# Performance work log

Measured on AMD Instinct MI355X. Metric: run time of the kernel, lower is better.

Reference implementation:

```python
import jax, jax.numpy as jnp
import numpy as np

OUT = 400          # resize target (tf.image.resize(img, [400, 400]))
THRESH = 0.7       # default threshold_value
B, H, W, C = 32, 512, 512, 3


def setup_inputs() -> dict:
    key = jax.random.key(0)
    k1, k2 = jax.random.split(key)
    image = jax.random.normal(k1, (B, H, W, C), dtype=jnp.float32)
    tensor = jax.random.uniform(k2, (B, H, W, 1), dtype=jnp.float32)
    return {"image": image, "tensor": tensor}


def _bounds(nz):
    # nz: bool [N]; first/last True index (tf.where(...)[0][0], [-1][0])
    n = nz.shape[0]
    first = jnp.argmax(nz).astype(jnp.int32)
    last = (n - 1 - jnp.argmax(nz[::-1])).astype(jnp.int32)
    return first, last


def _axis_coords(lo, hi, out):
    # TF2 bilinear resize: half-pixel centers, clamp into [0, size-1].
    # Crop is img[lo:hi] (exclusive hi, matching the TF slice semantics).
    size = (hi - lo).astype(jnp.float32)
    src = (jnp.arange(out, dtype=jnp.float32) + 0.5) * size / out - 0.5
    src = jnp.clip(src, 0.0, jnp.maximum(size - 1.0, 0.0))
    i0 = jnp.floor(src).astype(jnp.int32)
    i1 = jnp.minimum(i0 + 1, jnp.maximum(hi - lo - 1, 0))
    w = src - i0.astype(jnp.float32)
    return lo + i0, lo + i1, w  # absolute indices into the full image


def _crop_resize(img, msk):
    # img: [H, W, C]; msk: bool [H, W] == (tensor[..., 0] > THRESH)
    # rows: sum over axis=1 (tf sum_of_col), cols: sum over axis=0 (tf sum_of_row)
    left, right = _bounds(jnp.any(msk, axis=1))
    top, bot = _bounds(jnp.any(msk, axis=0))
    r0, r1, wr = _axis_coords(left, right, OUT)
    c0, c1, wc = _axis_coords(top, bot, OUT)
    a00 = img[r0[:, None], c0[None, :], :]
    a01 = img[r0[:, None], c1[None, :], :]
    a10 = img[r1[:, None], c0[None, :], :]
    a11 = img[r1[:, None], c1[None, :], :]
    wr_ = wr[:, None, None]
    wc_ = wc[None, :, None]
    top_i = a00 * (1.0 - wc_) + a01 * wc_
    bot_i = a10 * (1.0 - wc_) + a11 * wc_
    return top_i * (1.0 - wr_) + bot_i * wr_  # [OUT, OUT, C]


def reference(image, tensor):
    mask = tensor[..., 0] > THRESH
    return jax.vmap(_crop_resize)(image, mask)  # [B, 400, 400, C]
```

## Files before the change

kernel.cpp:

```cpp
#include <hip/hip_runtime.h>

#define OUTN 400
#define THRESH 0.7f
#define BB 32
#define HH 512
#define WW 512
#define CC 3
#define BIGI 0x7FFFFFFF

#define CHUNKS_PB 32
#define ROWS_PC   (HH / CHUNKS_PB)
#define PXPB      (OUTN * OUTN)
#define TPB       320
#define PXB       (TPB * 2)
#define BLKS_PB   (PXPB / PXB)
#define NXCD      8
#define RGRID     (BB * BLKS_PB)

typedef float vfloat4 __attribute__((ext_vector_type(4)));

__global__ void __launch_bounds__(256) bounds_part_kernel(
        const float* __restrict__ tensor,
        int4* __restrict__ part) {
    const int task  = blockIdx.x;
    const int b     = task >> 5;
    const int chunk = task & 31;

    const vfloat4* base = (const vfloat4*)(tensor + (size_t)b * HH * WW
                                                  + (size_t)chunk * ROWS_PC * WW);

    int minR = BIGI, maxR = -1, minC = BIGI, maxC = -1;

    #pragma unroll
    for (int it = 0; it < 8; ++it) {
        int p = threadIdx.x + it * 256;
        vfloat4 v = __builtin_nontemporal_load(base + p);
        int row  = p >> 7;
        int col0 = (p & 127) * 4;
        int mask = (v.x > THRESH ? 1 : 0) | (v.y > THRESH ? 2 : 0)
                 | (v.z > THRESH ? 4 : 0) | (v.w > THRESH ? 8 : 0);
        if (mask) {
            minR = min(minR, row);
            maxR = max(maxR, row);
            minC = min(minC, col0 + __builtin_ctz(mask));
            maxC = max(maxC, col0 + (31 - __builtin_clz(mask)));
        }
    }

    #pragma unroll
    for (int off = 32; off > 0; off >>= 1) {
        minR = min(minR, __shfl_down(minR, off));
        maxR = max(maxR, __shfl_down(maxR, off));
        minC = min(minC, __shfl_down(minC, off));
        maxC = max(maxC, __shfl_down(maxC, off));
    }

    __shared__ int s[4];
    if (threadIdx.x == 0) { s[0] = BIGI; s[1] = -1; s[2] = BIGI; s[3] = -1; }
    __syncthreads();
    if ((threadIdx.x & 63) == 0) {
        atomicMin(&s[0], minR); atomicMax(&s[1], maxR);
        atomicMin(&s[2], minC); atomicMax(&s[3], maxC);
    }
    __syncthreads();
    if (threadIdx.x == 0) {
        int4 r;
        if (s[1] >= 0) {
            r.x = s[0] + chunk * ROWS_PC;
            r.y = s[1] + chunk * ROWS_PC;
            r.z = s[2];
            r.w = s[3];
        } else {
            r.x = BIGI; r.y = -1; r.z = BIGI; r.w = -1;
        }
        part[task] = r;
    }
}

__device__ inline int4 fold_bounds(const int4* __restrict__ part, int b, int lane) {
    int4 p = part[b * CHUNKS_PB + (lane & 31)];
    #pragma unroll
    for (int off = 1; off < 32; off <<= 1) {
        p.x = min(p.x, __shfl_xor(p.x, off));
        p.y = max(p.y, __shfl_xor(p.y, off));
        p.z = min(p.z, __shfl_xor(p.z, off));
        p.w = max(p.w, __shfl_xor(p.w, off));
    }
    if (p.y < 0) { p.x = 0; p.y = HH - 1; }
    if (p.w < 0) { p.z = 0; p.w = WW - 1; }
    return p;
}

__device__ inline void ld3(const float* __restrict__ p, float* d) {
    d[0] = p[0]; d[1] = p[1]; d[2] = p[2];
}

__global__ void __launch_bounds__(TPB) resize_kernel(
        const float* __restrict__ img,
        const int4* __restrict__ part,
        float* __restrict__ out) {
    const int logical = (blockIdx.x % NXCD) * (RGRID / NXCD) + blockIdx.x / NXCD;

    const int t    = threadIdx.x;
    const int b    = logical / BLKS_PB;
    const int rem  = (logical % BLKS_PB) * PXB + t * 2;
    const int lane = t & 63;

    int4 f = fold_bounds(part, b, lane);
    const int minR = f.x, maxR = f.y, minC = f.z, maxC = f.w;

    const int ocol = rem % OUTN;
    const int orow = rem / OUTN;

    float sizeR = (float)(maxR - minR);
    float srcR  = ((float)orow + 0.5f) * sizeR * (1.0f / OUTN) - 0.5f;
    srcR = fminf(fmaxf(srcR, 0.0f), fmaxf(sizeR - 1.0f, 0.0f));
    int   i0 = (int)floorf(srcR);
    int   i1 = min(i0 + 1, max(maxR - minR - 1, 0));
    float wr = srcR - (float)i0;
    const int ro0 = (minR + i0) * (WW * CC);
    const int ro1 = (minR + i1) * (WW * CC);

    const float sizeC  = (float)(maxC - minC);
    const float hiClip = fmaxf(sizeC - 1.0f, 0.0f);
    const int   jmax   = max(maxC - minC - 1, 0);

    float srcC0 = ((float)ocol + 0.5f) * sizeC * (1.0f / OUTN) - 0.5f;
    srcC0 = fminf(fmaxf(srcC0, 0.0f), hiClip);
    int   j00 = (int)floorf(srcC0);
    int   j01 = min(j00 + 1, jmax);
    float wc0 = srcC0 - (float)j00;
    const int c00 = (minC + j00) * CC, c01 = (minC + j01) * CC;

    float srcC1 = ((float)ocol + 1.5f) * sizeC * (1.0f / OUTN) - 0.5f;
    srcC1 = fminf(fmaxf(srcC1, 0.0f), hiClip);
    int   j10 = (int)floorf(srcC1);
    int   j11 = min(j10 + 1, jmax);
    float wc1 = srcC1 - (float)j10;
    const int c10 = (minC + j10) * CC, c11 = (minC + j11) * CC;

    const float* __restrict__ ib = img + (size_t)b * (HH * WW * CC);

    float a00[3], a01[3], a10[3], a11[3];
    float d00[3], d01[3], d10[3], d11[3];
    ld3(ib + ro0 + c00, a00);
    ld3(ib + ro0 + c01, a01);
    ld3(ib + ro1 + c00, a10);
    ld3(ib + ro1 + c01, a11);
    ld3(ib + ro0 + c10, d00);
    ld3(ib + ro0 + c11, d01);
    ld3(ib + ro1 + c10, d10);
    ld3(ib + ro1 + c11, d11);

    float res[6];
    {
        float omc = 1.0f - wc0, omr = 1.0f - wr;
        #pragma unroll
        for (int ch = 0; ch < CC; ++ch) {
            float top = a00[ch] * omc + a01[ch] * wc0;
            float bot = a10[ch] * omc + a11[ch] * wc0;
            res[ch] = top * omr + bot * wr;
        }
        omc = 1.0f - wc1;
        #pragma unroll
        for (int ch = 0; ch < CC; ++ch) {
            float top = d00[ch] * omc + d01[ch] * wc1;
            float bot = d10[ch] * omc + d11[ch] * wc1;
            res[3 + ch] = top * omr + bot * wr;
        }
    }

    float* o = out + ((size_t)b * PXPB + (size_t)rem) * CC;
    #pragma unroll
    for (int i = 0; i < 6; ++i)
        __builtin_nontemporal_store(res[i], o + i);
}

extern "C" void kernel_launch(void* const* d_in, const int* in_sizes, int n_in,
                              void* d_out, int out_size, void* d_ws, size_t ws_size,
                              hipStream_t stream) {
    const float* image  = (const float*)d_in[0];
    const float* tensor = (const float*)d_in[1];
    float* out  = (float*)d_out;
    int4*  part = (int4*)d_ws;

    hipLaunchKernelGGL(bounds_part_kernel, dim3(BB * CHUNKS_PB), dim3(256), 0, stream,
                       tensor, part);

    hipLaunchKernelGGL(resize_kernel, dim3(RGRID), dim3(TPB), 0, stream,
                       image, part, out);
}
```

Baseline: 39.73 us.

## Stage source rows in LDS and compute row bands per block

The resize kernel now gives each block a band of 4 output rows. The block first cooperatively copies the 6 source image rows that band needs into shared memory with vector loads, and each thread then produces 5 consecutive output pixels from LDS. This replaces scattered per-pixel global gathers with coalesced row loads plus LDS reads, aiming to cut redundant global and L2 traffic. In exchange it adds a block-wide barrier, uses about 36 KB of LDS per block, which limits occupancy, and always loads full-width rows even when the crop is narrow.

```diff
diff --git a/kernel.cpp b/kernel.cpp
--- a/kernel.cpp
+++ b/kernel.cpp
@@ -12,10 +12,12 @@
 #define ROWS_PC   (HH / CHUNKS_PB)
 #define PXPB      (OUTN * OUTN)
 #define TPB       320
-#define PXB       (TPB * 2)
-#define BLKS_PB   (PXPB / PXB)
+#define ROWS_PBLK 4
+#define BANDS_PB  (OUTN / ROWS_PBLK)
+#define RGRID     (BB * BANDS_PB)
 #define NXCD      8
-#define RGRID     (BB * BLKS_PB)
+#define SROWS     6
+#define ROWF      (WW * CC)
 
 typedef float vfloat4 __attribute__((ext_vector_type(4)));
 
@@ -91,88 +93,75 @@
     return p;
 }
 
-__device__ inline void ld3(const float* __restrict__ p, float* d) {
-    d[0] = p[0]; d[1] = p[1]; d[2] = p[2];
-}
-
 __global__ void __launch_bounds__(TPB) resize_kernel(
         const float* __restrict__ img,
         const int4* __restrict__ part,
         float* __restrict__ out) {
     const int logical = (blockIdx.x % NXCD) * (RGRID / NXCD) + blockIdx.x / NXCD;
+    const int t     = threadIdx.x;
+    const int b     = logical / BANDS_PB;
+    const int orow0 = (logical % BANDS_PB) * ROWS_PBLK;
 
-    const int t    = threadIdx.x;
-    const int b    = logical / BLKS_PB;
-    const int rem  = (logical % BLKS_PB) * PXB + t * 2;
-    const int lane = t & 63;
-
-    int4 f = fold_bounds(part, b, lane);
+    int4 f = fold_bounds(part, b, t & 63);
     const int minR = f.x, maxR = f.y, minC = f.z, maxC = f.w;
 
-    const int ocol = rem % OUTN;
-    const int orow = rem / OUTN;
+    const float sizeR  = (float)(maxR - minR);
+    const float hiClpR = fmaxf(sizeR - 1.0f, 0.0f);
+    const int   imaxR  = max(maxR - minR - 1, 0);
 
-    float sizeR = (float)(maxR - minR);
-    float srcR  = ((float)orow + 0.5f) * sizeR * (1.0f / OUTN) - 0.5f;
-    srcR = fminf(fmaxf(srcR, 0.0f), fmaxf(sizeR - 1.0f, 0.0f));
+    float s0 = ((float)orow0 + 0.5f) * sizeR / (float)OUTN - 0.5f;
+    s0 = fminf(fmaxf(s0, 0.0f), hiClpR);
+    int rstart = minR + (int)floorf(s0);
+    rstart = min(rstart, HH - SROWS);
+
+    __shared__ float lds[SROWS * ROWF];
+
+    {
+        const vfloat4* src = (const vfloat4*)(img + (size_t)b * (HH * ROWF)
+                                                  + (size_t)rstart * ROWF);
+        vfloat4* dst = (vfloat4*)lds;
+        for (int p = t; p < SROWS * (ROWF / 4); p += TPB)
+            dst[p] = src[p];
+    }
+    __syncthreads();
+
+    const int row   = orow0 + t / 80;
+    const int ocol0 = (t % 80) * 5;
+
+    float srcR = ((float)row + 0.5f) * sizeR / (float)OUTN - 0.5f;
+    srcR = fminf(fmaxf(srcR, 0.0f), hiClpR);
     int   i0 = (int)floorf(srcR);
-    int   i1 = min(i0 + 1, max(maxR - minR - 1, 0));
+    int   i1 = min(i0 + 1, imaxR);
     float wr = srcR - (float)i0;
-    const int ro0 = (minR + i0) * (WW * CC);
-    const int ro1 = (minR + i1) * (WW * CC);
+    const float* __restrict__ row0 = lds + (size_t)(minR + i0 - rstart) * ROWF;
+    const float* __restrict__ row1 = lds + (size_t)(minR + i1 - rstart) * ROWF;
+    const float omr = 1.0f - wr;
 
     const float sizeC  = (float)(maxC - minC);
-    const float hiClip = fmaxf(sizeC - 1.0f, 0.0f);
-    const int   jmax   = max(maxC - minC - 1, 0);
+    const float hiClpC = fmaxf(sizeC - 1.0f, 0.0f);
+    const int   jmaxC  = max(maxC - minC - 1, 0);
 
-    float srcC0 = ((float)ocol + 0.5f) * sizeC * (1.0f / OUTN) - 0.5f;
-    srcC0 = fminf(fmaxf(srcC0, 0.0f), hiClip);
-    int   j00 = (int)floorf(srcC0);
-    int   j01 = min(j00 + 1, jmax);
-    float wc0 = srcC0 - (float)j00;
-    const int c00 = (minC + j00) * CC, c01 = (minC + j01) * CC;
-
-    float srcC1 = ((float)ocol + 1.5f) * sizeC * (1.0f / OUTN) - 0.5f;
-    srcC1 = fminf(fmaxf(srcC1, 0.0f), hiClip);
-    int   j10 = (int)floorf(srcC1);
-    int   j11 = min(j10 + 1, jmax);
-    float wc1 = srcC1 - (float)j10;
-    const int c10 = (minC + j10) * CC, c11 = (minC + j11) * CC;
-
-    const float* __restrict__ ib = img + (size_t)b * (HH * WW * CC);
-
-    float a00[3], a01[3], a10[3], a11[3];
-    float d00[3], d01[3], d10[3], d11[3];
-    ld3(ib + ro0 + c00, a00);
-    ld3(ib + ro0 + c01, a01);
-    ld3(ib + ro1 + c00, a10);
-    ld3(ib + ro1 + c01, a11);
-    ld3(ib + ro0 + c10, d00);
-    ld3(ib + ro0 + c11, d01);
-    ld3(ib + ro1 + c10, d10);
-    ld3(ib + ro1 + c11, d11);
-
-    float res[6];
-    {
-        float omc = 1.0f - wc0, omr = 1.0f - wr;
+    float res[15];
+    #pragma unroll
+    for (int k = 0; k < 5; ++k) {
+        float srcC = ((float)(ocol0 + k) + 0.5f) * sizeC / (float)OUTN - 0.5f;
+        srcC = fminf(fmaxf(srcC, 0.0f), hiClpC);
+        int   j0 = (int)floorf(srcC);
+        int   j1 = min(j0 + 1, jmaxC);
+        float wc = srcC - (float)j0;
+        int c0 = (minC + j0) * CC, c1 = (minC + j1) * CC;
+        float omc = 1.0f - wc;
         #pragma unroll
         for (int ch = 0; ch < CC; ++ch) {
-            float top = a00[ch] * omc + a01[ch] * wc0;
-            float bot = a10[ch] * omc + a11[ch] * wc0;
-            res[ch] = top * omr + bot * wr;
-        }
-        omc = 1.0f - wc1;
-        #pragma unroll
-        for (int ch = 0; ch < CC; ++ch) {
-            float top = d00[ch] * omc + d01[ch] * wc1;
-            float bot = d10[ch] * omc + d11[ch] * wc1;
-            res[3 + ch] = top * omr + bot * wr;
+            float top = row0[c0 + ch] * omc + row0[c1 + ch] * wc;
+            float bot = row1[c0 + ch] * omc + row1[c1 + ch] * wc;
+            res[k * 3 + ch] = top * omr + bot * wr;
         }
     }
 
-    float* o = out + ((size_t)b * PXPB + (size_t)rem) * CC;
+    float* o = out + ((size_t)b * PXPB + (size_t)row * OUTN + ocol0) * CC;
     #pragma unroll
-    for (int i = 0; i < 6; ++i)
+    for (int i = 0; i < 15; ++i)
         __builtin_nontemporal_store(res[i], o + i);
 }
 
```

Result: slower. 59.11 us (+48.8%).
